# Performance work log

Measured on AMD Instinct MI355X. Metric: run time of the kernel, lower is better.

## Reference

```python
import jax, jax.numpy as jnp
import numpy as np

N_NODES = 100000
N_EDGES = 600000
D = 128
N_TYPES = 3


def setup_inputs() -> dict:
    key = jax.random.key(0)
    ks = jax.random.split(key, 10)
    x = jax.random.normal(ks[0], (N_NODES, D), dtype=jnp.float32)
    edge_index = jax.random.randint(ks[1], (2, N_EDGES), 0, N_NODES, dtype=jnp.int64)
    edge_type_ids = jax.random.randint(ks[2], (N_EDGES,), 0, N_TYPES, dtype=jnp.int32)
    edge_weights = jax.random.uniform(ks[3], (N_EDGES,), dtype=jnp.float32)
    # Xavier-uniform linear weights (in==out==D), zero biases, uniform attention
    limit = float(np.sqrt(6.0 / (D + D)))
    W_edge = jax.random.uniform(ks[4], (N_TYPES, D, D), minval=-limit, maxval=limit, dtype=jnp.float32)
    b_edge = jnp.zeros((N_TYPES, D), dtype=jnp.float32)
    W_self = jax.random.uniform(ks[5], (D, D), minval=-limit, maxval=limit, dtype=jnp.float32)
    b_self = jnp.zeros((D,), dtype=jnp.float32)
    attention = jnp.ones((N_TYPES + 1,), dtype=jnp.float32) / (N_TYPES + 1)
    return {"x": x, "edge_index": edge_index, "edge_type_ids": edge_type_ids,
            "edge_weights": edge_weights, "W_edge": W_edge, "b_edge": b_edge,
            "W_self": W_self, "b_self": b_self, "attention": attention}


def reference(x, edge_index, edge_type_ids, edge_weights, W_edge, b_edge, W_self, b_self, attention):
    n_nodes = x.shape[0]
    n_types = W_edge.shape[0]
    src, dst = edge_index[0], edge_index[1]
    xs = x[src]  # (E, D) gather once, shared by all edge types
    outs = []
    for t in range(n_types):  # small fixed set of structurally distinct linears
        # mask zeros out edges of other types; equivalent to torch's boolean slicing
        m = jnp.where(edge_type_ids == t, edge_weights, jnp.zeros((), x.dtype))
        y = (xs @ W_edge[t] + b_edge[t]) * m[:, None]  # (E, D)
        outs.append(jax.ops.segment_sum(y, dst, num_segments=n_nodes))  # scatter-add
    outs.append(x @ W_self + b_self)
    stacked = jnp.stack(outs, axis=-1)  # (N, D, n_types+1)
    attn = jax.nn.softmax(attention)
    out = jnp.sum(stacked * attn, axis=-1)
    return jax.nn.gelu(out, approximate=False)  # torch F.gelu default is erf-based
```

## Files before the change

### kernel.cpp

```cpp
#include <hip/hip_runtime.h>
#include <hip/hip_bf16.h>
#include <math.h>

#define D 128
#define NT 3
#define KTOT (D * (NT + 1))
#define TM 32
#define NCAP 32

typedef __attribute__((ext_vector_type(8))) __bf16 bf16x8;
typedef __attribute__((ext_vector_type(4))) float f32x4;

__device__ inline unsigned short f2bf(float f) {
    unsigned int u = __float_as_uint(f);
    unsigned int r = (u + 0x7FFFu + ((u >> 16) & 1u)) >> 16;
    return (unsigned short)r;
}
__device__ inline float bf2f(unsigned int low16) {
    return __uint_as_float(low16 << 16);
}

__global__ void zero_kernel(float* __restrict__ p, long long n4) {
    long long i = (long long)blockIdx.x * blockDim.x + threadIdx.x;
    long long stride = (long long)gridDim.x * blockDim.x;
    float4 z = make_float4(0.f, 0.f, 0.f, 0.f);
    for (; i < n4; i += stride) ((float4*)p)[i] = z;
}

__global__ void prep_kernel(const float* __restrict__ W_edge, const float* __restrict__ b_edge,
                            const float* __restrict__ W_self, const float* __restrict__ b_self,
                            const float* __restrict__ attention,
                            float* __restrict__ wcat, float* __restrict__ biasb,
                            unsigned short* __restrict__ bfrag,
                            int* __restrict__ zeroMe, int zeroN) {
    float a0 = attention[0], a1 = attention[1], a2 = attention[2], a3 = attention[3];
    float m = fmaxf(fmaxf(a0, a1), fmaxf(a2, a3));
    float e0 = expf(a0 - m), e1 = expf(a1 - m), e2 = expf(a2 - m), e3 = expf(a3 - m);
    float inv = 1.f / (e0 + e1 + e2 + e3);
    float at[4] = {e0 * inv, e1 * inv, e2 * inv, e3 * inv};

    int idx0 = blockIdx.x * blockDim.x + threadIdx.x;
    int stride = gridDim.x * blockDim.x;
    if (zeroMe) {
        for (int i = idx0; i < zeroN; i += stride) zeroMe[i] = 0;
    }
    for (int i = idx0; i < KTOT * D; i += stride) {
        int k = i >> 7, j = i & (D - 1);
        float v;
        if (k < D) {
            v = at[NT] * W_self[k * D + j];
        } else {
            int t = (k - D) >> 7;
            int kk = (k - D) & (D - 1);
            v = at[t] * W_edge[(t * D + kk) * D + j];
        }
        wcat[i] = v;
    }
    for (int i = idx0; i < KTOT; i += stride) {
        if (i < NT * D) {
            int t = i >> 7, j = i & (D - 1);
            biasb[i] = at[t] * b_edge[t * D + j];
        } else {
            biasb[i] = at[NT] * b_self[i - NT * D];
        }
    }
    if (bfrag) {
        for (int i = idx0; i < 16 * 8 * 64; i += stride) {
            int l = i & 63;
            int cf = (i >> 6) & 7;
            int step = i >> 9;
            int col = cf * 16 + (l & 15);
            int kb = step * 32 + ((l >> 4) * 8);
#pragma unroll
            for (int j = 0; j < 8; ++j) {
                int k = kb + j;
                float v;
                if (k < D) {
                    v = at[NT] * W_self[k * D + col];
                } else {
                    int t = (k - D) >> 7;
                    int kk = (k - D) & (D - 1);
                    v = at[t] * W_edge[(t * D + kk) * D + col];
                }
                bfrag[(size_t)i * 8 + j] = f2bf(v);
            }
        }
    }
}

__global__ __launch_bounds__(256) void xcvt_kernel(
    const float* __restrict__ x, unsigned short* __restrict__ xb, int nN) {
    int i = blockIdx.x * blockDim.x + threadIdx.x;
    int total = nN * (D / 4);
    int stride = gridDim.x * blockDim.x;
    for (; i < total; i += stride) {
        int n = i >> 5;
        int c4 = (i & 31) * 4;
        float4 v = *(const float4*)(x + (size_t)n * D + c4);
        ushort4 o;
        o.x = f2bf(v.x); o.y = f2bf(v.y); o.z = f2bf(v.z); o.w = f2bf(v.w);
        *(ushort4*)(xb + (size_t)n * D + c4) = o;
    }
}

__global__ __launch_bounds__(256) void fill_kernel(
    const int* __restrict__ ei, const int* __restrict__ et, const float* __restrict__ ew,
    int* __restrict__ deg, int2* __restrict__ csr, int* __restrict__ ovfcnt,
    int* __restrict__ ovflist, int nE) {
    int e = blockIdx.x * blockDim.x + threadIdx.x;
    if (e >= nE) return;
    int dst = ei[nE + e];
    int pos = atomicAdd(deg + dst, 1);
    if (pos < NCAP) {
        int src = ei[e];
        int t = et[e];
        csr[(size_t)dst * NCAP + pos] = make_int2(src | (t << 20), __float_as_int(ew[e]));
    } else {
        int o = atomicAdd(ovfcnt, 1);
        ovflist[o] = e;
    }
}

__global__ __launch_bounds__(512, 6) void fused_gemm_kernel(
    const unsigned short* __restrict__ xb, const int2* __restrict__ csr,
    const int* __restrict__ deg, const unsigned short* __restrict__ bfrag,
    const float* __restrict__ biasb,
    const int* __restrict__ ei, const int* __restrict__ et, const float* __restrict__ ew,
    const int* __restrict__ ovfc, const int* __restrict__ ovfl,
    float* __restrict__ out, int nN, int nE) {
    __shared__ unsigned char lds[49536];
    float* sL = (float*)(lds + 49152);
    int t = threadIdx.x;
    int w = t >> 6;
    int lane = t & 63;
    int gl = lane & 15;
    int gbase = lane & 48;
    int row0 = blockIdx.x * TM;

#define BSTAGE(buf, st_) do {                                                                     \
        const unsigned short* gsrc = bfrag + (size_t)(st_) * 4096 + w * 512 + lane * 8;           \
        unsigned char* ldst = lds + 32768 + (buf) * 8192 + w * 1024;                              \
        __builtin_amdgcn_global_load_lds((const __attribute__((address_space(1))) void*)gsrc,     \
                                         (__attribute__((address_space(3))) void*)ldst, 16, 0, 0);\
    } while (0)

    BSTAGE(0, 0);

    int lrow = w * 4 + (lane >> 4);
    int node = row0 + lrow;
    int nclamp = (node < nN) ? node : (nN - 1);
    int dg = (node < nN) ? deg[nclamp] : 0;
    if (dg > NCAP) dg = NCAP;
    const int2* c = csr + (size_t)nclamp * NCAP;
    int2 mA = (gl < dg) ? c[gl] : make_int2(0, 0);
    int2 mB = (gl + 16 < dg) ? c[gl + 16] : make_int2(0, 0);

    float ac0[8], ac1[8], ac2[8];
#pragma unroll
    for (int j = 0; j < 8; ++j) { ac0[j] = 0.f; ac1[j] = 0.f; ac2[j] = 0.f; }
    float sw0 = 0.f, sw1 = 0.f, sw2 = 0.f;

    for (int i = 0; i < dg; i += 2) {
        int slA = gbase + (i & 15);
        int exA = __shfl((i < 16) ? mA.x : mB.x, slA);
        int ewA = __shfl((i < 16) ? mA.y : mB.y, slA);
        int srcA = exA & 0xFFFFF;
        if (srcA >= nN) srcA = 0;
        float wA = __int_as_float(ewA);
        int tA = (exA >> 20) & 3;
        bool actB = (i + 1 < dg);
        int slB = gbase + ((i + 1) & 15);
        int exB = __shfl((i + 1 < 16) ? mA.x : mB.x, slB);
        int ewB = __shfl((i + 1 < 16) ? mA.y : mB.y, slB);
        int srcB = exB & 0xFFFFF;
        if (!actB || srcB >= nN) srcB = 0;
        float wB = actB ? __int_as_float(ewB) : 0.f;
        int tB = (exB >> 20) & 3;

        uint4 xa = *(const uint4*)(xb + (size_t)srcA * D + gl * 8);
        uint4 xv = *(const uint4*)(xb + (size_t)srcB * D + gl * 8);

        float wA0 = (tA == 0) ? wA : 0.f;
        float wA1 = (tA == 1) ? wA : 0.f;
        float wA2 = (tA == 2) ? wA : 0.f;
        float wB0 = (tB == 0) ? wB : 0.f;
        float wB1 = (tB == 1) ? wB : 0.f;
        float wB2 = (tB == 2) ? wB : 0.f;
        sw0 += wA0 + wB0; sw1 += wA1 + wB1; sw2 += wA2 + wB2;

        float f0, f1;
#define ACCUM(u, j0, j1, w0_, w1_, w2_)                                   \
        f0 = __uint_as_float((u) << 16);                                  \
        f1 = __uint_as_float((u) & 0xFFFF0000u);                          \
        ac0[j0] = fmaf(w0_, f0, ac0[j0]); ac0[j1] = fmaf(w0_, f1, ac0[j1]); \
        ac1[j0] = fmaf(w1_, f0, ac1[j0]); ac1[j1] = fmaf(w1_, f1, ac1[j1]); \
        ac2[j0] = fmaf(w2_, f0, ac2[j0]); ac2[j1] = fmaf(w2_, f1, ac2[j1]);
        ACCUM(xa.x, 0, 1, wA0, wA1, wA2)
        ACCUM(xa.y, 2, 3, wA0, wA1, wA2)
        ACCUM(xa.z, 4, 5, wA0, wA1, wA2)
        ACCUM(xa.w, 6, 7, wA0, wA1, wA2)
        ACCUM(xv.x, 0, 1, wB0, wB1, wB2)
        ACCUM(xv.y, 2, 3, wB0, wB1, wB2)
        ACCUM(xv.z, 4, 5, wB0, wB1, wB2)
        ACCUM(xv.w, 6, 7, wB0, wB1, wB2)
#undef ACCUM
    }

    {
        int swz = lrow & 15;
        uint4 xo = *(const uint4*)(xb + (size_t)nclamp * D + gl * 8);
        *(uint4*)(lds + lrow * 1024 + ((gl ^ swz) << 4)) = xo;
        uint4 o;
#define PACKST(arr, tt)                                                                \
        o.x = (unsigned int)f2bf(arr[0]) | ((unsigned int)f2bf(arr[1]) << 16);         \
        o.y = (unsigned int)f2bf(arr[2]) | ((unsigned int)f2bf(arr[3]) << 16);         \
        o.z = (unsigned int)f2bf(arr[4]) | ((unsigned int)f2bf(arr[5]) << 16);         \
        o.w = (unsigned int)f2bf(arr[6]) | ((unsigned int)f2bf(arr[7]) << 16);         \
        *(uint4*)(lds + lrow * 1024 + 256 + (tt) * 256 + ((gl ^ swz) << 4)) = o;
        PACKST(ac0, 0)
        PACKST(ac1, 1)
        PACKST(ac2, 2)
#undef PACKST
        if (gl < 3) {
            float sv = (gl == 0) ? sw0 : ((gl == 1) ? sw1 : sw2);
            sL[lrow * NT + gl] = sv;
        }
    }
    __syncthreads();

    int cnt = *ovfc;
    if (cnt > 0) {
        if (w == 0 && lane < 16) {
            for (int i = 0; i < cnt; ++i) {
                int e = ovfl[i];
                int dst = ei[nE + e];
                if (dst >= row0 && dst < row0 + TM && dst < nN) {
                    int tt = et[e];
                    float wt = ew[e];
                    int src = ei[e];
                    int lr = dst - row0;
                    uint4* p = (uint4*)(lds + lr * 1024 + 256 + tt * 256 + ((lane ^ (lr & 15)) << 4));
                    uint4 cu = *p;
                    uint4 xr = *(const uint4*)(xb + (size_t)src * D + lane * 8);
                    float f0 = bf2f(cu.x & 0xFFFF) + wt * bf2f(xr.x & 0xFFFF);
                    float f1 = bf2f(cu.x >> 16)    + wt * bf2f(xr.x >> 16);
                    float f2 = bf2f(cu.y & 0xFFFF) + wt * bf2f(xr.y & 0xFFFF);
                    float f3 = bf2f(cu.y >> 16)    + wt * bf2f(xr.y >> 16);
                    float f4 = bf2f(cu.z & 0xFFFF) + wt * bf2f(xr.z & 0xFFFF);
                    float f5 = bf2f(cu.z >> 16)    + wt * bf2f(xr.z >> 16);
                    float f6 = bf2f(cu.w & 0xFFFF) + wt * bf2f(xr.w & 0xFFFF);
                    float f7 = bf2f(cu.w >> 16)    + wt * bf2f(xr.w >> 16);
                    cu.x = (unsigned int)f2bf(f0) | ((unsigned int)f2bf(f1) << 16);
                    cu.y = (unsigned int)f2bf(f2) | ((unsigned int)f2bf(f3) << 16);
                    cu.z = (unsigned int)f2bf(f4) | ((unsigned int)f2bf(f5) << 16);
                    cu.w = (unsigned int)f2bf(f6) | ((unsigned int)f2bf(f7) << 16);
                    *p = cu;
                    if (lane == 0) sL[lr * NT + tt] += wt;
                }
            }
        }
        __syncthreads();
    }

    int ll = lane & 15;
    int ck = lane >> 4;
    f32x4 acc0 = (f32x4){0.f, 0.f, 0.f, 0.f};
    f32x4 acc1 = (f32x4){0.f, 0.f, 0.f, 0.f};
#pragma unroll 2
    for (int st = 0; st < 16; ++st) {
        int cur = st & 1;
        if (st < 15) BSTAGE(cur ^ 1, st + 1);
        int cc = st * 4 + ck;
        int phys = (cc & 48) | ((cc & 15) ^ ll);
        bf16x8 a0 = *(const bf16x8*)(lds + ll * 1024 + (phys << 4));
        bf16x8 a1 = *(const bf16x8*)(lds + (16 + ll) * 1024 + (phys << 4));
        bf16x8 b = *(const bf16x8*)(lds + 32768 + cur * 8192 + ((w * 64 + lane) << 4));
        acc0 = __builtin_amdgcn_mfma_f32_16x16x32_bf16(a0, b, acc0, 0, 0, 0);
        acc1 = __builtin_amdgcn_mfma_f32_16x16x32_bf16(a1, b, acc1, 0, 0, 0);
        __syncthreads();
    }
#undef BSTAGE

    int colb = w * 16 + ll;
    float bb0 = biasb[colb], bb1 = biasb[D + colb], bb2 = biasb[2 * D + colb], bs4 = biasb[3 * D + colb];
    const float kInvSqrt2 = 0.70710678118654752440f;
#pragma unroll
    for (int fr = 0; fr < 2; ++fr) {
        f32x4 A = fr ? acc1 : acc0;
#pragma unroll
        for (int reg = 0; reg < 4; ++reg) {
            int lr = fr * 16 + ck * 4 + reg;
            long row = (long)row0 + lr;
            if (row >= nN) continue;
            float s0 = sL[lr * NT + 0];
            float s1 = sL[lr * NT + 1];
            float s2 = sL[lr * NT + 2];
            float v = A[reg] + bs4 + s0 * bb0 + s1 * bb1 + s2 * bb2;
            v = 0.5f * v * (1.f + erff(v * kInvSqrt2));
            out[row * D + colb] = v;
        }
    }
}

__global__ __launch_bounds__(256) void scatterA_kernel(
    const float* __restrict__ x, const int* __restrict__ ei,
    const int* __restrict__ et, const float* __restrict__ ew,
    float* __restrict__ agg, float* __restrict__ s, int nE) {
    int gtid = blockIdx.x * blockDim.x + threadIdx.x;
    int wave = gtid >> 6;
    int lane = threadIdx.x & 63;
    int nw = (gridDim.x * blockDim.x) >> 6;
    for (int e = wave; e < nE; e += nw) {
        int src = ei[e];
        int dst = ei[nE + e];
        int t = et[e];
        float w = ew[e];
        float2 xv = *(const float2*)(x + (size_t)src * D + lane * 2);
        float* p = agg + (size_t)dst * (NT * D) + t * D + lane * 2;
        unsafeAtomicAdd(p, w * xv.x);
        unsafeAtomicAdd(p + 1, w * xv.y);
        if (lane == 0) unsafeAtomicAdd(s + (size_t)dst * NT + t, w);
    }
}

#define BM 64
#define BK 32
__global__ __launch_bounds__(256) void gemm_gelu_kernel(
    const float* __restrict__ x, const float* __restrict__ agg,
    const float* __restrict__ s, const float* __restrict__ wcat,
    const float* __restrict__ biasb, float* __restrict__ out, int nNodes) {
    __shared__ float As[BK][BM + 1];
    __shared__ float Bs[BK][D];

    int tx = threadIdx.x;
    int row0 = blockIdx.x * BM;
    int cg = tx & 31;
    int rg = tx >> 5;
    int lr = tx >> 3;
    int lc = (tx & 7) * 4;

    float acc[8][4];
#pragma unroll
    for (int i = 0; i < 8; ++i)
#pragma unroll
        for (int j = 0; j < 4; ++j) acc[i][j] = 0.f;

    for (int k0 = 0; k0 < KTOT; k0 += BK) {
        const float* srcBase;
        int strideA, koff;
        if (k0 < D) { srcBase = x; strideA = D; koff = k0; }
        else        { srcBase = agg; strideA = NT * D; koff = k0 - D; }
#pragma unroll
        for (int h = 0; h < 2; ++h) {
            int r = lr + h * 32;
            int node = row0 + r;
            if (node >= nNodes) node = nNodes - 1;
            float4 v = *(const float4*)(srcBase + (size_t)node * strideA + koff + lc);
            As[lc + 0][r] = v.x; As[lc + 1][r] = v.y;
            As[lc + 2][r] = v.z; As[lc + 3][r] = v.w;
        }
        {
            int br = tx >> 5;
            int bc = (tx & 31) * 4;
#pragma unroll
            for (int h = 0; h < 4; ++h) {
                int r = br + h * 8;
                *(float4*)(&Bs[r][bc]) = *(const float4*)(wcat + (size_t)(k0 + r) * D + bc);
            }
        }
        __syncthreads();
#pragma unroll
        for (int kk = 0; kk < BK; ++kk) {
            float4 b = *(const float4*)(&Bs[kk][cg * 4]);
            float a[8];
            *(float4*)(a)     = *(const float4*)(&As[kk][rg * 8]);
            *(float4*)(a + 4) = *(const float4*)(&As[kk][rg * 8 + 4]);
#pragma unroll
            for (int i = 0; i < 8; ++i) {
                acc[i][0] = fmaf(a[i], b.x, acc[i][0]);
                acc[i][1] = fmaf(a[i], b.y, acc[i][1]);
                acc[i][2] = fmaf(a[i], b.z, acc[i][2]);
                acc[i][3] = fmaf(a[i], b.w, acc[i][3]);
            }
        }
        __syncthreads();
    }

    int jc = cg * 4;
    float4 bb0 = *(const float4*)(biasb + 0 * D + jc);
    float4 bb1 = *(const float4*)(biasb + 1 * D + jc);
    float4 bb2 = *(const float4*)(biasb + 2 * D + jc);
    float4 bsv = *(const float4*)(biasb + NT * D + jc);
#pragma unroll
    for (int i = 0; i < 8; ++i) {
        int node = row0 + rg * 8 + i;
        if (node >= nNodes) break;
        float s0 = s[(size_t)node * NT + 0];
        float s1 = s[(size_t)node * NT + 1];
        float s2 = s[(size_t)node * NT + 2];
        float4 r;
        r.x = acc[i][0] + bsv.x + s0 * bb0.x + s1 * bb1.x + s2 * bb2.x;
        r.y = acc[i][1] + bsv.y + s0 * bb0.y + s1 * bb1.y + s2 * bb2.y;
        r.z = acc[i][2] + bsv.z + s0 * bb0.z + s1 * bb1.z + s2 * bb2.z;
        r.w = acc[i][3] + bsv.w + s0 * bb0.w + s1 * bb1.w + s2 * bb2.w;
        const float kInvSqrt2 = 0.70710678118654752440f;
        r.x = 0.5f * r.x * (1.f + erff(r.x * kInvSqrt2));
        r.y = 0.5f * r.y * (1.f + erff(r.y * kInvSqrt2));
        r.z = 0.5f * r.z * (1.f + erff(r.z * kInvSqrt2));
        r.w = 0.5f * r.w * (1.f + erff(r.w * kInvSqrt2));
        *(float4*)(out + (size_t)node * D + jc) = r;
    }
}

__global__ __launch_bounds__(256) void selfmv_kernel(
    const float* __restrict__ x, const float* __restrict__ Ws,
    const float* __restrict__ bs, const float* __restrict__ attn,
    float* __restrict__ out, int nN) {
    float a0 = attn[0], a1 = attn[1], a2 = attn[2], a3 = attn[3];
    float m = fmaxf(fmaxf(a0, a1), fmaxf(a2, a3));
    float e3 = expf(a3 - m);
    float inv = 1.f / (expf(a0 - m) + expf(a1 - m) + expf(a2 - m) + e3);
    float at3 = e3 * inv;
    int wave = (blockIdx.x * blockDim.x + threadIdx.x) >> 6;
    int lane = threadIdx.x & 63;
    int nw = (gridDim.x * blockDim.x) >> 6;
    for (int n = wave; n < nN; n += nw) {
        float2 xr = *(const float2*)(x + (size_t)n * D + lane * 2);
        float acc0 = 0.f, acc1 = 0.f;
#pragma unroll
        for (int k = 0; k < D; ++k) {
            float xv = __shfl((k & 1) ? xr.y : xr.x, k >> 1);
            float2 wv = *(const float2*)(Ws + (size_t)k * D + lane * 2);
            acc0 = fmaf(xv, wv.x, acc0);
            acc1 = fmaf(xv, wv.y, acc1);
        }
        float2 r;
        r.x = at3 * (acc0 + bs[lane * 2]);
        r.y = at3 * (acc1 + bs[lane * 2 + 1]);
        *(float2*)(out + (size_t)n * D + lane * 2) = r;
    }
}

__global__ __launch_bounds__(256) void edgemv_kernel(
    const float* __restrict__ x, const int* __restrict__ ei,
    const int* __restrict__ et, const float* __restrict__ ew,
    const float* __restrict__ We, const float* __restrict__ be,
    const float* __restrict__ attn, float* __restrict__ out, int nE) {
    float a0 = attn[0], a1 = attn[1], a2 = attn[2], a3 = attn[3];
    float m = fmaxf(fmaxf(a0, a1), fmaxf(a2, a3));
    float e0 = expf(a0 - m), e1 = expf(a1 - m), e2 = expf(a2 - m), e3 = expf(a3 - m);
    float inv = 1.f / (e0 + e1 + e2 + e3);
    float at[NT] = {e0 * inv, e1 * inv, e2 * inv};
    int wave = (blockIdx.x * blockDim.x + threadIdx.x) >> 6;
    int lane = threadIdx.x & 63;
    int nw = (gridDim.x * blockDim.x) >> 6;
    for (int e = wave; e < nE; e += nw) {
        int src = ei[e];
        int dst = ei[nE + e];
        int t = et[e];
        float sc = ew[e] * at[t];
        const float* W = We + (size_t)t * D * D;
        float2 xr = *(const float2*)(x + (size_t)src * D + lane * 2);
        float acc0 = 0.f, acc1 = 0.f;
#pragma unroll
        for (int k = 0; k < D; ++k) {
            float xv = __shfl((k & 1) ? xr.y : xr.x, k >> 1);
            float2 wv = *(const float2*)(W + (size_t)k * D + lane * 2);
            acc0 = fmaf(xv, wv.x, acc0);
            acc1 = fmaf(xv, wv.y, acc1);
        }
        float* p = out + (size_t)dst * D + lane * 2;
        unsafeAtomicAdd(p,     sc * (acc0 + be[(size_t)t * D + lane * 2]));
        unsafeAtomicAdd(p + 1, sc * (acc1 + be[(size_t)t * D + lane * 2 + 1]));
    }
}

__global__ void gelu_kernel(float* __restrict__ p, long long n4) {
    long long i = (long long)blockIdx.x * blockDim.x + threadIdx.x;
    long long stride = (long long)gridDim.x * blockDim.x;
    const float kInvSqrt2 = 0.70710678118654752440f;
    for (; i < n4; i += stride) {
        float4 r = ((float4*)p)[i];
        r.x = 0.5f * r.x * (1.f + erff(r.x * kInvSqrt2));
        r.y = 0.5f * r.y * (1.f + erff(r.y * kInvSqrt2));
        r.z = 0.5f * r.z * (1.f + erff(r.z * kInvSqrt2));
        r.w = 0.5f * r.w * (1.f + erff(r.w * kInvSqrt2));
        ((float4*)p)[i] = r;
    }
}

extern "C" void kernel_launch(void* const* d_in, const int* in_sizes, int n_in,
                              void* d_out, int out_size, void* d_ws, size_t ws_size,
                              hipStream_t stream) {
    const float* x = (const float*)d_in[0];
    const int* ei = (const int*)d_in[1];
    const int* et = (const int*)d_in[2];
    const float* ew = (const float*)d_in[3];
    const float* W_edge = (const float*)d_in[4];
    const float* b_edge = (const float*)d_in[5];
    const float* W_self = (const float*)d_in[6];
    const float* b_self = (const float*)d_in[7];
    const float* attention = (const float*)d_in[8];
    float* out = (float*)d_out;

    const int nN = in_sizes[0] / D;
    const int nE = in_sizes[2];

    size_t off = 0;
    auto take = [&](size_t bytes) { size_t o = (off + 15) & ~(size_t)15; off = o + bytes; return o; };
    size_t o_wcat  = take((size_t)KTOT * D * 4);
    size_t o_biasb = take((size_t)KTOT * 4);
    size_t o_bfrag = take(131072);
    size_t o_deg   = take((size_t)(nN + 2) * 4);
    size_t o_ovfl  = take((size_t)nE * 4);
    size_t o_csr   = take((size_t)nN * NCAP * 8);
    size_t o_xb    = take((size_t)nN * D * 2);
    size_t needFused = off;

    if (ws_size >= needFused && nN < (1 << 20)) {
        char* ws = (char*)d_ws;
        float* wcat = (float*)(ws + o_wcat);
        float* biasb = (float*)(ws + o_biasb);
        unsigned short* bfrag = (unsigned short*)(ws + o_bfrag);
        int* deg = (int*)(ws + o_deg);
        int* ovfc = deg + nN;
        int* ovfl = (int*)(ws + o_ovfl);
        int2* csr = (int2*)(ws + o_csr);
        unsigned short* xb = (unsigned short*)(ws + o_xb);

        hipLaunchKernelGGL(prep_kernel, dim3(64), dim3(256), 0, stream,
                           W_edge, b_edge, W_self, b_self, attention, wcat, biasb, bfrag,
                           deg, nN + 2);
        hipLaunchKernelGGL(xcvt_kernel, dim3(2048), dim3(256), 0, stream, x, xb, nN);
        hipLaunchKernelGGL(fill_kernel, dim3((nE + 255) / 256), dim3(256), 0, stream,
                           ei, et, ew, deg, csr, ovfc, ovfl, nE);
        hipLaunchKernelGGL(fused_gemm_kernel, dim3((nN + TM - 1) / TM), dim3(512), 0, stream,
                           xb, csr, deg, bfrag, biasb, ei, et, ew, ovfc, ovfl, out, nN, nE);
        return;
    }

    const size_t baseFloats = (size_t)nN * NT * D + (size_t)nN * NT + (size_t)KTOT * D + KTOT;
    if (ws_size >= baseFloats * 4) {
        float* agg = (float*)d_ws;
        float* sW = agg + (size_t)nN * NT * D;
        float* wcat = sW + (size_t)nN * NT;
        float* biasb = wcat + (size_t)KTOT * D;
        long long zeroFloats = (long long)nN * (NT * D + NT);
        hipLaunchKernelGGL(zero_kernel, dim3(2048), dim3(256), 0, stream, agg, (zeroFloats + 3) / 4);
        hipLaunchKernelGGL(prep_kernel, dim3(64), dim3(256), 0, stream,
                           W_edge, b_edge, W_self, b_self, attention, wcat, biasb,
                           (unsigned short*)nullptr, (int*)nullptr, 0);
        hipLaunchKernelGGL(scatterA_kernel, dim3(2048), dim3(256), 0, stream,
                           x, ei, et, ew, agg, sW, nE);
        hipLaunchKernelGGL(gemm_gelu_kernel, dim3((nN + BM - 1) / BM), dim3(256), 0, stream,
                           x, agg, sW, wcat, biasb, out, nN);
    } else {
        hipLaunchKernelGGL(selfmv_kernel, dim3(2048), dim3(256), 0, stream,
                           x, W_self, b_self, attention, out, nN);
        hipLaunchKernelGGL(edgemv_kernel, dim3(2048), dim3(256), 0, stream,
                           x, ei, et, ew, W_edge, b_edge, attention, out, nE);
        hipLaunchKernelGGL(gelu_kernel, dim3(2048), dim3(256), 0, stream,
                           out, (long long)nN * D / 4);
    }
}
```

Baseline: 125.9 us.

## Fuse x conversion with CSR fill and read B fragments directly from global

Merges the bf16 conversion of x and the edge-bucketing fill into one kernel launch, with each thread loading its edge before the conversion loop so the load latency overlaps. In the GEMM stage, B fragments are now read straight from global memory (cached) instead of being staged through double-buffered LDS, which removes the per-step __syncthreads and 16KB of LDS. The smaller LDS footprint lets launch bounds rise to 8 blocks per SM. The cost is B reads hitting cache or global memory on every step instead of LDS, plus higher register pressure under the tighter occupancy bound.

```diff
diff --git a/kernel.cpp b/kernel.cpp
--- a/kernel.cpp
+++ b/kernel.cpp
@@ -88,12 +88,26 @@
     }
 }
 
-__global__ __launch_bounds__(256) void xcvt_kernel(
-    const float* __restrict__ x, unsigned short* __restrict__ xb, int nN) {
-    int i = blockIdx.x * blockDim.x + threadIdx.x;
+__global__ __launch_bounds__(256) void xcvt_fill_kernel(
+    const float* __restrict__ x, unsigned short* __restrict__ xb, int nN,
+    const int* __restrict__ ei, const int* __restrict__ et, const float* __restrict__ ew,
+    int* __restrict__ deg, int2* __restrict__ csr, int* __restrict__ ovfcnt,
+    int* __restrict__ ovflist, int nE) {
+    int e = blockIdx.x * blockDim.x + threadIdx.x;
+
+    int dst = 0, src = 0, t = 0;
+    float w = 0.f;
+    bool act = (e < nE);
+    if (act) {
+        dst = ei[nE + e];
+        src = ei[e];
+        t = et[e];
+        w = ew[e];
+    }
+
     int total = nN * (D / 4);
     int stride = gridDim.x * blockDim.x;
-    for (; i < total; i += stride) {
+    for (int i = e; i < total; i += stride) {
         int n = i >> 5;
         int c4 = (i & 31) * 4;
         float4 v = *(const float4*)(x + (size_t)n * D + c4);
@@ -101,50 +115,33 @@
         o.x = f2bf(v.x); o.y = f2bf(v.y); o.z = f2bf(v.z); o.w = f2bf(v.w);
         *(ushort4*)(xb + (size_t)n * D + c4) = o;
     }
-}
-
-__global__ __launch_bounds__(256) void fill_kernel(
-    const int* __restrict__ ei, const int* __restrict__ et, const float* __restrict__ ew,
-    int* __restrict__ deg, int2* __restrict__ csr, int* __restrict__ ovfcnt,
-    int* __restrict__ ovflist, int nE) {
-    int e = blockIdx.x * blockDim.x + threadIdx.x;
-    if (e >= nE) return;
-    int dst = ei[nE + e];
-    int pos = atomicAdd(deg + dst, 1);
-    if (pos < NCAP) {
-        int src = ei[e];
-        int t = et[e];
-        csr[(size_t)dst * NCAP + pos] = make_int2(src | (t << 20), __float_as_int(ew[e]));
-    } else {
-        int o = atomicAdd(ovfcnt, 1);
-        ovflist[o] = e;
-    }
-}
-
-__global__ __launch_bounds__(512, 6) void fused_gemm_kernel(
+
+    if (act) {
+        int pos = atomicAdd(deg + dst, 1);
+        if (pos < NCAP) {
+            csr[(size_t)dst * NCAP + pos] = make_int2(src | (t << 20), __float_as_int(w));
+        } else {
+            int o = atomicAdd(ovfcnt, 1);
+            ovflist[o] = e;
+        }
+    }
+}
+
+__global__ __launch_bounds__(512, 8) void fused_gemm_kernel(
     const unsigned short* __restrict__ xb, const int2* __restrict__ csr,
     const int* __restrict__ deg, const unsigned short* __restrict__ bfrag,
     const float* __restrict__ biasb,
     const int* __restrict__ ei, const int* __restrict__ et, const float* __restrict__ ew,
     const int* __restrict__ ovfc, const int* __restrict__ ovfl,
     float* __restrict__ out, int nN, int nE) {
-    __shared__ unsigned char lds[49536];
-    float* sL = (float*)(lds + 49152);
+    __shared__ unsigned char lds[33152];
+    float* sL = (float*)(lds + 32768);
     int t = threadIdx.x;
     int w = t >> 6;
     int lane = t & 63;
     int gl = lane & 15;
     int gbase = lane & 48;
     int row0 = blockIdx.x * TM;
-
-#define BSTAGE(buf, st_) do {                                                                     \
-        const unsigned short* gsrc = bfrag + (size_t)(st_) * 4096 + w * 512 + lane * 8;           \
-        unsigned char* ldst = lds + 32768 + (buf) * 8192 + w * 1024;                              \
-        __builtin_amdgcn_global_load_lds((const __attribute__((address_space(1))) void*)gsrc,     \
-                                         (__attribute__((address_space(3))) void*)ldst, 16, 0, 0);\
-    } while (0)
-
-    BSTAGE(0, 0);
 
     int lrow = w * 4 + (lane >> 4);
     int node = row0 + lrow;
@@ -266,20 +263,16 @@
     int ck = lane >> 4;
     f32x4 acc0 = (f32x4){0.f, 0.f, 0.f, 0.f};
     f32x4 acc1 = (f32x4){0.f, 0.f, 0.f, 0.f};
-#pragma unroll 2
+#pragma unroll 4
     for (int st = 0; st < 16; ++st) {
-        int cur = st & 1;
-        if (st < 15) BSTAGE(cur ^ 1, st + 1);
+        bf16x8 b = *(const bf16x8*)(bfrag + (size_t)st * 4096 + w * 512 + lane * 8);
         int cc = st * 4 + ck;
         int phys = (cc & 48) | ((cc & 15) ^ ll);
         bf16x8 a0 = *(const bf16x8*)(lds + ll * 1024 + (phys << 4));
         bf16x8 a1 = *(const bf16x8*)(lds + (16 + ll) * 1024 + (phys << 4));
-        bf16x8 b = *(const bf16x8*)(lds + 32768 + cur * 8192 + ((w * 64 + lane) << 4));
         acc0 = __builtin_amdgcn_mfma_f32_16x16x32_bf16(a0, b, acc0, 0, 0, 0);
         acc1 = __builtin_amdgcn_mfma_f32_16x16x32_bf16(a1, b, acc1, 0, 0, 0);
-        __syncthreads();
-    }
-#undef BSTAGE
+    }
 
     int colb = w * 16 + ll;
     float bb0 = biasb[colb], bb1 = biasb[D + colb], bb2 = biasb[2 * D + colb], bs4 = biasb[3 * D + colb];
@@ -531,9 +524,8 @@
         hipLaunchKernelGGL(prep_kernel, dim3(64), dim3(256), 0, stream,
                            W_edge, b_edge, W_self, b_self, attention, wcat, biasb, bfrag,
                            deg, nN + 2);
-        hipLaunchKernelGGL(xcvt_kernel, dim3(2048), dim3(256), 0, stream, x, xb, nN);
-        hipLaunchKernelGGL(fill_kernel, dim3((nE + 255) / 256), dim3(256), 0, stream,
-                           ei, et, ew, deg, csr, ovfc, ovfl, nE);
+        hipLaunchKernelGGL(xcvt_fill_kernel, dim3((nE + 255) / 256), dim3(256), 0, stream,
+                           x, xb, nN, ei, et, ew, deg, csr, ovfc, ovfl, nE);
         hipLaunchKernelGGL(fused_gemm_kernel, dim3((nN + TM - 1) / TM), dim3(512), 0, stream,
                            xb, csr, deg, bfrag, biasb, ei, et, ew, ovfc, ovfl, out, nN, nE);
         return;
```

Measured after the change: 117.4 us. 6.7% less time.
